# Optimization experiments

Measured on AMD Instinct MI355X. Metric: run time of the kernel, lower is better.

Reference implementation:

```python
import jax, jax.numpy as jnp
import numpy as np

D_MODEL = 512
NUM_HEADS = 8
QUERY_GROUPS = 2
HEAD_DIM = D_MODEL // NUM_HEADS  # 64
ROPE_THETA = 10000.0
SCALE = 0.125  # 1/sqrt(head_dim)
NEG_INF = -1e9


def setup_inputs() -> dict:
    key = jax.random.key(0)
    k1, k2, k3 = jax.random.split(key, 3)
    B, T, S = 2, 512, 16
    x = jax.random.normal(k1, (B, T, S, D_MODEL), jnp.float32)
    padding_mask = jnp.ones((B, T * S), jnp.int32)  # [B, T*H*W], all valid
    qkv_dim = NUM_HEADS * HEAD_DIM + 2 * QUERY_GROUPS * HEAD_DIM  # 768
    qkv_w = jax.random.normal(k2, (qkv_dim, D_MODEL), jnp.float32) / np.float32(np.sqrt(D_MODEL))
    o_w = jax.random.normal(k3, (D_MODEL, NUM_HEADS * HEAD_DIM), jnp.float32) / np.float32(np.sqrt(D_MODEL))
    return {"x": x, "padding_mask": padding_mask, "qkv_w": qkv_w, "o_w": o_w}


def _rope(v, pos):
    # v: [N, T, h, d]; classic RoPE (rotate-half) over temporal positions
    half = v.shape[-1] // 2
    inv_freq = 1.0 / (ROPE_THETA ** (jnp.arange(0, half, dtype=jnp.float32) / half))
    ang = pos[:, None] * inv_freq  # [T, half]
    cos = jnp.cos(ang)[None, :, None, :]
    sin = jnp.sin(ang)[None, :, None, :]
    v1, v2 = v[..., :half], v[..., half:]
    return jnp.concatenate([v1 * cos - v2 * sin, v1 * sin + v2 * cos], axis=-1)


def reference(x, padding_mask, qkv_w, o_w):
    B, T, S, D = x.shape
    # temporal attention: flatten spatial patches into batch -> [B*S, T, D]
    xt = x.transpose(0, 2, 1, 3).reshape(B * S, T, D)
    qkv = xt @ qkv_w.T  # [B*S, T, (H+2G)*hd]
    q_end = NUM_HEADS * HEAD_DIM
    k_end = q_end + QUERY_GROUPS * HEAD_DIM
    q = qkv[..., :q_end].reshape(B * S, T, NUM_HEADS, HEAD_DIM)
    k = qkv[..., q_end:k_end].reshape(B * S, T, QUERY_GROUPS, HEAD_DIM)
    v = qkv[..., k_end:].reshape(B * S, T, QUERY_GROUPS, HEAD_DIM)
    pos = jnp.arange(T, dtype=jnp.float32)
    q = _rope(q, pos)
    k = _rope(k, pos)
    # GQA: broadcast each KV group to its query heads
    rep = NUM_HEADS // QUERY_GROUPS
    k = jnp.repeat(k, rep, axis=2)
    v = jnp.repeat(v, rep, axis=2)
    scores = jnp.einsum('nqhd,nkhd->nhqk', q, k) * SCALE  # [B*S, H, T, T]
    causal = jnp.tril(jnp.ones((T, T), bool))
    pm = padding_mask.astype(bool).reshape(-1, T)  # [B*S, T] query-side mask (as in torch path)
    mask = causal[None, None, :, :] & pm[:, None, :, None]
    scores = jnp.where(mask, scores, NEG_INF)
    attn = jax.nn.softmax(scores, axis=-1)
    out = jnp.einsum('nhqk,nkhd->nqhd', attn, v).reshape(B * S, T, D)
    out = out @ o_w.T  # output projection
    return out.reshape(B, S, T, D).transpose(0, 2, 1, 3)  # back to [B, T, S, D]
```

## Files before the change

kernel.cpp:

```cpp
#include <hip/hip_runtime.h>
#include <hip/hip_bf16.h>

typedef __attribute__((ext_vector_type(8))) short bf16x8;
typedef __attribute__((ext_vector_type(4))) float f32x4;
typedef __attribute__((ext_vector_type(4))) short s16x4;

#define DM 512
#define T_SEQ 512
#define NSEQ 32
#define MROWS 16384
#define QKV_DIM 768
#define HD 64
#define NEG_INF_F (-1000000000.0f)
#define LOG2E 1.44269504088896340736f

__device__ __forceinline__ short f2bf(float f) {
    unsigned int u = __builtin_bit_cast(unsigned int, f);
    unsigned int r = (u + 0x7FFFu + ((u >> 16) & 1u)) >> 16;
    return (short)r;
}

__device__ __forceinline__ short f2bf_hw(float f) {
    __hip_bfloat16 h = __float2bfloat16(f);
    return __builtin_bit_cast(short, h);
}

__device__ __forceinline__ void gload16(const void* g, void* l) {
    __builtin_amdgcn_global_load_lds(
        (const __attribute__((address_space(1))) void*)g,
        (__attribute__((address_space(3))) void*)l, 16, 0, 0);
}

__global__ __launch_bounds__(128) void k_convert(
    const float* __restrict__ x, const float* __restrict__ qkvw, const float* __restrict__ owf,
    short* __restrict__ xt, short* __restrict__ qw, short* __restrict__ ow,
    float* __restrict__ cosT, float* __restrict__ sinT)
{
    int bidx = blockIdx.x, tid = threadIdx.x;
    if (bidx < MROWS) {
        int m = bidx; int n = m >> 9, t = m & 511, b = n >> 4, s = n & 15;
        const float* src = x + ((size_t)((b * 512 + t) * 16 + s)) * 512;
        float4 v = *(const float4*)(src + tid * 4);
        s16x4 o; o.x = f2bf(v.x); o.y = f2bf(v.y); o.z = f2bf(v.z); o.w = f2bf(v.w);
        *(s16x4*)(xt + (size_t)m * 512 + tid * 4) = o;
    } else if (bidx < MROWS + 1280) {
        int wr = bidx - MROWS;
        const float* src; short* dst;
        if (wr < QKV_DIM) { src = qkvw + (size_t)wr * 512; dst = qw + (size_t)wr * 512; }
        else             { src = owf + (size_t)(wr - QKV_DIM) * 512; dst = ow + (size_t)(wr - QKV_DIM) * 512; }
        float4 v = *(const float4*)(src + tid * 4);
        s16x4 o; o.x = f2bf(v.x); o.y = f2bf(v.y); o.z = f2bf(v.z); o.w = f2bf(v.w);
        *(s16x4*)(dst + tid * 4) = o;
    } else {
        int idx = (bidx - (MROWS + 1280)) * 128 + tid;
        int t = idx >> 5, d = idx & 31;
        float inv = powf(10000.0f, -(float)d * (1.0f / 32.0f));
        float ang = (float)t * inv;
        float sv, cv; sincosf(ang, &sv, &cv);
        cosT[idx] = cv; sinT[idx] = sv;
    }
}

__device__ __forceinline__ void gemm_mainloop_db(
    const short* __restrict__ Ab, const short* __restrict__ Bb, int K,
    short* As0, short* As1, short* Bs0, short* Bs1,
    int wave, int lane, f32x4 acc[4][4])
{
    int wr = (wave >> 1) * 64, wc = (wave & 1) * 64;
    int cl = lane & 15, g = lane >> 4;
    auto stg = [&](int kt, short* As, short* Bs) {
        #pragma unroll
        for (int c = 0; c < 2; ++c) {
            int chunk = (wave * 2 + c) * 64 + lane;
            int row = chunk >> 2, kc = chunk & 3;
            gload16(Ab + (size_t)row * K + kt + kc * 8, As + (wave * 2 + c) * 512);
            gload16(Bb + (size_t)row * K + kt + kc * 8, Bs + (wave * 2 + c) * 512);
        }
    };
    stg(0, As0, Bs0);
    for (int kt = 0; kt < K; kt += 32) {
        short* Asc = (kt & 32) ? As1 : As0;
        short* Bsc = (kt & 32) ? Bs1 : Bs0;
        short* Asn = (kt & 32) ? As0 : As1;
        short* Bsn = (kt & 32) ? Bs0 : Bs1;
        __syncthreads();
        if (kt + 32 < K) stg(kt + 32, Asn, Bsn);
        bf16x8 af[4], bg[4];
        #pragma unroll
        for (int mf = 0; mf < 4; ++mf)
            af[mf] = *(const bf16x8*)(Asc + (wr + mf * 16 + cl) * 32 + (g << 3));
        #pragma unroll
        for (int nf = 0; nf < 4; ++nf)
            bg[nf] = *(const bf16x8*)(Bsc + (wc + nf * 16 + cl) * 32 + (g << 3));
        #pragma unroll
        for (int mf = 0; mf < 4; ++mf)
            #pragma unroll
            for (int nf = 0; nf < 4; ++nf)
                acc[mf][nf] = __builtin_amdgcn_mfma_f32_16x16x32_bf16(af[mf], bg[nf], acc[mf][nf], 0, 0, 0);
    }
}

__global__ __launch_bounds__(256) void k_gemm_qkv(
    const short* __restrict__ xt, const short* __restrict__ qw,
    const float* __restrict__ cosT, const float* __restrict__ sinT,
    short* __restrict__ qb, short* __restrict__ kb, short* __restrict__ vtb)
{
    __shared__ short As0[128 * 32], As1[128 * 32], Bs0[128 * 32], Bs1[128 * 32];
    __shared__ short Vld[4][16 * 64];
    int tid = threadIdx.x, wave = tid >> 6, lane = tid & 63;
    int cl = lane & 15, g = lane >> 4;
    int o = blockIdx.x;
    int swz = (o & 7) * 96 + (o >> 3);
    int bm = swz / 6, bn = swz % 6;
    f32x4 acc[4][4] = {};
    gemm_mainloop_db(xt + (size_t)bm * 128 * 512, qw + (size_t)bn * 128 * 512, 512,
                     As0, As1, Bs0, Bs1, wave, lane, acc);

    const float QSC = 0.125f * LOG2E;
    int wr = (wave >> 1) * 64, wc = (wave & 1) * 64;
    int gbase = bn * 128 + wc;

    if (gbase < 640) {
        #pragma unroll
        for (int mf = 0; mf < 4; ++mf) {
            #pragma unroll
            for (int rg = 0; rg < 4; ++rg) {
                int r = bm * 128 + wr + mf * 16 + (g << 2) + rg;
                int n = r >> 9, t = r & 511;
                #pragma unroll
                for (int nf = 0; nf < 2; ++nf) {
                    int dlo = nf * 16 + cl;
                    float v1 = acc[mf][nf][rg];
                    float v2 = acc[mf][nf + 2][rg];
                    float c = cosT[t * 32 + dlo], s = sinT[t * 32 + dlo];
                    if (gbase < 512) {
                        int h = gbase >> 6;
                        size_t base = ((size_t)(n * 8 + h) * 512 + t) * 64;
                        qb[base + dlo]      = f2bf_hw((v1 * c - v2 * s) * QSC);
                        qb[base + dlo + 32] = f2bf_hw((v1 * s + v2 * c) * QSC);
                    } else {
                        int gk = (gbase - 512) >> 6;
                        size_t base = ((size_t)(n * 2 + gk) * 512 + t) * 64;
                        kb[base + dlo]      = f2bf_hw(v1 * c - v2 * s);
                        kb[base + dlo + 32] = f2bf_hw(v1 * s + v2 * c);
                    }
                }
            }
        }
    } else {
        int gq = (gbase - 640) >> 6;
        #pragma unroll
        for (int mf = 0; mf < 4; ++mf) {
            #pragma unroll
            for (int nf = 0; nf < 2; ++nf) {
                int dlo = nf * 16 + cl;
                s16x4 plo, phi;
                #pragma unroll
                for (int rg = 0; rg < 4; ++rg) {
                    ((short*)&plo)[rg] = f2bf_hw(acc[mf][nf][rg]);
                    ((short*)&phi)[rg] = f2bf_hw(acc[mf][nf + 2][rg]);
                }
                *(s16x4*)(&Vld[wave][dlo * 16 + (g << 2)])        = plo;
                *(s16x4*)(&Vld[wave][(dlo + 32) * 16 + (g << 2)]) = phi;
            }
            int r0 = bm * 128 + wr + mf * 16;
            int n = r0 >> 9, t0 = r0 & 511;
            size_t vb = ((size_t)(n * 2 + gq) * 64 + lane) * 512;
            bf16x8 va = *(const bf16x8*)(&Vld[wave][lane * 16]);
            bf16x8 vb8 = *(const bf16x8*)(&Vld[wave][lane * 16 + 8]);
            *(bf16x8*)(vtb + vb + t0)     = va;
            *(bf16x8*)(vtb + vb + t0 + 8) = vb8;
        }
    }
}

__global__ __launch_bounds__(512) void k_attn(
    const short* __restrict__ qb, const short* __restrict__ kb, const short* __restrict__ vtb,
    const int* __restrict__ pm, short* __restrict__ ao)
{
    __shared__ short Kt[2][64 * 64];
    __shared__ short Vt[2][64 * 64];
    __shared__ short Pws[8][16 * 64];
    int tid = threadIdx.x, wave = tid >> 6, lane = tid & 63;
    int cl = lane & 15, g = lane >> 4;
    int o = blockIdx.x;
    int swz = (o & 7) * 64 + (o >> 3);
    int c = swz & 3, hp = (swz >> 2) & 3, n = swz >> 4;
    int kg = hp >> 1;
    int h = hp * 2 + (wave >> 2);
    int u = wave & 3;
    const short* Qb = qb + ((size_t)(n * 8 + h) * 512) * 64;
    const short* Kb = kb + ((size_t)(n * 2 + kg) * 512) * 64;
    const short* Vb = vtb + ((size_t)(n * 2 + kg) * 64) * 512;

    auto stage = [&](int jt, int buf) {
        int c0 = jt * 64;
        int chunk = wave * 64 + lane;
        int row = chunk >> 3, kc = chunk & 7;
        int sw = (kc ^ (row & 7)) << 3;
        gload16(Kb + (size_t)(c0 + row) * 64 + sw, &Kt[buf][wave * 512]);
        gload16(Vb + (size_t)row * 512 + c0 + sw, &Vt[buf][wave * 512]);
    };

    stage(0, 0);
    int buf = 0;
    #pragma unroll
    for (int ph = 0; ph < 2; ++ph) {
        int rowb = (ph ? (7 - c) : c) * 64 + u * 16;
        int NTp = ph ? (8 - c) : (c + 1);
        bf16x8 qf[2];
        #pragma unroll
        for (int ks = 0; ks < 2; ++ks)
            qf[ks] = *(const bf16x8*)(Qb + (size_t)(rowb + cl) * 64 + ks * 32 + (g << 3));
        f32x4 Oc[4] = {};
        float mrow = -1e30f, lrow = 0.f;
        bool rv = pm[n * 512 + rowb + cl] != 0;
        int rq = rowb + cl;

        for (int jt = 0; jt < NTp; ++jt) {
            __syncthreads();
            if (jt + 1 < NTp) stage(jt + 1, buf ^ 1);
            else if (ph == 0) stage(0, buf ^ 1);
            int c0 = jt * 64;
            const short* Kc = Kt[buf];
            const short* Vc = Vt[buf];
            buf ^= 1;

            f32x4 sacc[4] = {};
            #pragma unroll
            for (int ks = 0; ks < 2; ++ks) {
                #pragma unroll
                for (int nf = 0; nf < 4; ++nf) {
                    int row = nf * 16 + cl;
                    int kc = ks * 4 + g;
                    bf16x8 kf = *(const bf16x8*)(Kc + row * 64 + ((kc ^ (row & 7)) << 3));
                    sacc[nf] = __builtin_amdgcn_mfma_f32_16x16x32_bf16(kf, qf[ks], sacc[nf], 0, 0, 0);
                }
            }

            const bool diag = (jt == NTp - 1);
            float rmax = -1e30f;
            if (diag) {
                #pragma unroll
                for (int nf = 0; nf < 4; ++nf)
                    #pragma unroll
                    for (int rg = 0; rg < 4; ++rg) {
                        int kv = c0 + nf * 16 + g * 4 + rg;
                        float sv = sacc[nf][rg];
                        sv = (kv <= rq && rv) ? sv : NEG_INF_F;
                        sacc[nf][rg] = sv;
                        rmax = fmaxf(rmax, sv);
                    }
            } else {
                #pragma unroll
                for (int nf = 0; nf < 4; ++nf)
                    #pragma unroll
                    for (int rg = 0; rg < 4; ++rg)
                        rmax = fmaxf(rmax, sacc[nf][rg]);
            }
            rmax = fmaxf(rmax, __shfl_xor(rmax, 16));
            rmax = fmaxf(rmax, __shfl_xor(rmax, 32));
            float mold = mrow;
            int defer = __all(rmax - mold <= 8.0f);
            float mnew = defer ? mold : fmaxf(mold, rmax);
            mrow = mnew;
            float rsum = 0.f;
            #pragma unroll
            for (int nf = 0; nf < 4; ++nf) {
                s16x4 pk;
                #pragma unroll
                for (int rg = 0; rg < 4; ++rg) {
                    float p = exp2f(sacc[nf][rg] - mnew);
                    rsum += p;
                    ((short*)&pk)[rg] = f2bf_hw(p);
                }
                *(s16x4*)(&Pws[wave][cl * 64 + ((((nf << 1) + (g >> 1)) ^ (cl & 7)) << 3) + ((g & 1) << 2)]) = pk;
            }
            rsum += __shfl_xor(rsum, 16);
            rsum += __shfl_xor(rsum, 32);
            if (defer) {
                lrow += rsum;
            } else {
                float alpha = exp2f(mold - mnew);
                lrow = lrow * alpha + rsum;
                #pragma unroll
                for (int rg = 0; rg < 4; ++rg) {
                    float av = __shfl(alpha, (lane & 48) + (g << 2) + rg);
                    #pragma unroll
                    for (int nf = 0; nf < 4; ++nf) Oc[nf][rg] *= av;
                }
            }

            #pragma unroll
            for (int ks = 0; ks < 2; ++ks) {
                bf16x8 pf = *(const bf16x8*)(&Pws[wave][cl * 64 + (((ks * 4 + g) ^ (cl & 7)) << 3)]);
                #pragma unroll
                for (int nf = 0; nf < 4; ++nf) {
                    int row = nf * 16 + cl;
                    int kc = ks * 4 + g;
                    bf16x8 vf = *(const bf16x8*)(Vc + row * 64 + ((kc ^ (row & 7)) << 3));
                    Oc[nf] = __builtin_amdgcn_mfma_f32_16x16x32_bf16(pf, vf, Oc[nf], 0, 0, 0);
                }
            }
        }

        #pragma unroll
        for (int rg = 0; rg < 4; ++rg) {
            float li = __shfl(lrow, (lane & 48) + (g << 2) + rg);
            float inv = 1.0f / li;
            int r = rowb + g * 4 + rg;
            size_t base = ((size_t)n * 512 + r) * 512 + h * 64;
            #pragma unroll
            for (int nf = 0; nf < 4; ++nf)
                ao[base + nf * 16 + cl] = f2bf_hw(Oc[nf][rg] * inv);
        }
    }
}

__global__ __launch_bounds__(256) void k_gemm_out(
    const short* __restrict__ ao, const short* __restrict__ ow, float* __restrict__ out)
{
    __shared__ short As0[128 * 32], As1[128 * 32], Bs0[128 * 32], Bs1[128 * 32];
    int tid = threadIdx.x, wave = tid >> 6, lane = tid & 63;
    int o = blockIdx.x;
    int swz = (o & 7) * 64 + (o >> 3);
    int bm = swz >> 2, bn = swz & 3;
    f32x4 acc[4][4] = {};
    gemm_mainloop_db(ao + (size_t)bm * 128 * 512, ow + (size_t)bn * 128 * 512, 512,
                     As0, As1, Bs0, Bs1, wave, lane, acc);

    int wr = (wave >> 1) * 64, wc = (wave & 1) * 64;
    #pragma unroll
    for (int mf = 0; mf < 4; ++mf) {
        #pragma unroll
        for (int rg = 0; rg < 4; ++rg) {
            int r = bm * 128 + wr + mf * 16 + ((lane >> 4) << 2) + rg;
            int n = r >> 9, t = r & 511, b = n >> 4, s = n & 15;
            size_t obase = ((size_t)((b * 512 + t) * 16 + s)) * 512;
            #pragma unroll
            for (int nf = 0; nf < 4; ++nf) {
                int ccc = bn * 128 + wc + nf * 16 + (lane & 15);
                out[obase + ccc] = acc[mf][nf][rg];
            }
        }
    }
}

extern "C" void kernel_launch(void* const* d_in, const int* in_sizes, int n_in,
                              void* d_out, int out_size, void* d_ws, size_t ws_size,
                              hipStream_t stream) {
    (void)in_sizes; (void)n_in; (void)out_size; (void)ws_size;
    const float* x    = (const float*)d_in[0];
    const int*   pmsk = (const int*)d_in[1];
    const float* qkvw = (const float*)d_in[2];
    const float* owf  = (const float*)d_in[3];
    char* ws = (char*)d_ws;
    short* xt   = (short*)(ws + 0);
    short* qw   = (short*)(ws + 16777216);
    short* ow   = (short*)(ws + 17563648);
    float* cosT = (float*)(ws + 18087936);
    float* sinT = (float*)(ws + 18153472);
    short* qbuf = (short*)(ws + 18219008);
    short* kbuf = (short*)(ws + 34996224);
    short* vtbuf= (short*)(ws + 39190528);
    short* aobuf = xt;
    float* out = (float*)d_out;

    k_convert<<<dim3(17792), dim3(128), 0, stream>>>(x, qkvw, owf, xt, qw, ow, cosT, sinT);
    k_gemm_qkv<<<dim3(768), dim3(256), 0, stream>>>(xt, qw, cosT, sinT, qbuf, kbuf, vtbuf);
    k_attn<<<dim3(512), dim3(512), 0, stream>>>(qbuf, kbuf, vtbuf, pmsk, aobuf);
    k_gemm_out<<<dim3(512), dim3(256), 0, stream>>>(aobuf, ow, out);
}
```

Baseline: 79.10 us.

## Rewrite QKV GEMM with 256x256 tiles, 8 waves, swizzled LDS, ping-pong pipeline

```diff
diff --git a/kernel.cpp b/kernel.cpp
--- a/kernel.cpp
+++ b/kernel.cpp
@@ -100,32 +100,127 @@
     }
 }
 
-__global__ __launch_bounds__(256) void k_gemm_qkv(
+__global__ __launch_bounds__(512) void k_gemm_qkv(
     const short* __restrict__ xt, const short* __restrict__ qw,
     const float* __restrict__ cosT, const float* __restrict__ sinT,
     short* __restrict__ qb, short* __restrict__ kb, short* __restrict__ vtb)
 {
-    __shared__ short As0[128 * 32], As1[128 * 32], Bs0[128 * 32], Bs1[128 * 32];
-    __shared__ short Vld[4][16 * 64];
+    __shared__ short lds[65536];
     int tid = threadIdx.x, wave = tid >> 6, lane = tid & 63;
     int cl = lane & 15, g = lane >> 4;
     int o = blockIdx.x;
-    int swz = (o & 7) * 96 + (o >> 3);
-    int bm = swz / 6, bn = swz % 6;
-    f32x4 acc[4][4] = {};
-    gemm_mainloop_db(xt + (size_t)bm * 128 * 512, qw + (size_t)bn * 128 * 512, 512,
-                     As0, As1, Bs0, Bs1, wave, lane, acc);
+    int swz = (o & 7) * 24 + (o >> 3);
+    int bm = swz / 3, bn = swz % 3;
+    const short* Ag = xt + (size_t)bm * 256 * 512;
+    const short* Bg = qw + (size_t)bn * 256 * 512;
+
+    int r0 = tid >> 3, kc0 = tid & 7;
+    int r1 = 64 + (tid >> 3);
+    auto stage = [&](int mat, int half, int tile, int buf) {
+        const short* gb = mat ? Bg : Ag;
+        short* lb = lds + mat * 32768 + buf * 16384 + half * 8192;
+        int kt = tile * 64;
+        gload16(gb + (size_t)(half * 128 + r0) * 512 + kt + ((kc0 ^ (r0 & 7)) << 3), lb + tid * 8);
+        gload16(gb + (size_t)(half * 128 + r1) * 512 + kt + ((kc0 ^ (r1 & 7)) << 3), lb + 4096 + tid * 8);
+    };
+
+    stage(1, 0, 0, 0); stage(1, 1, 0, 0); stage(0, 0, 0, 0); stage(0, 1, 0, 0);
+    stage(1, 0, 1, 1); stage(1, 1, 1, 1);
+
+    int wA = (wave >> 2) * 128, wB = (wave & 3) * 64;
+    int cs0 = g ^ (cl & 7);
+    int cs1 = cs0 ^ 4;
+    f32x4 acc[8][4] = {};
+    bf16x8 af[4][2], bg[4][2];
+
+    for (int k = 0; k < 8; ++k) {
+        int buf = k & 1;
+        const short* Ab = lds + buf * 16384;
+        const short* Bb = lds + 32768 + buf * 16384;
+        if (k < 7) stage(0, 0, k + 1, buf ^ 1);
+        asm volatile("s_waitcnt vmcnt(6)" ::: "memory");
+        __builtin_amdgcn_s_barrier();
+        __builtin_amdgcn_sched_barrier(0);
+        #pragma unroll
+        for (int mf = 0; mf < 4; ++mf) {
+            af[mf][0] = *(const bf16x8*)(Ab + (wA + mf * 16 + cl) * 64 + cs0 * 8);
+            af[mf][1] = *(const bf16x8*)(Ab + (wA + mf * 16 + cl) * 64 + cs1 * 8);
+        }
+        #pragma unroll
+        for (int nf = 0; nf < 2; ++nf) {
+            bg[nf][0] = *(const bf16x8*)(Bb + (wB + nf * 16 + cl) * 64 + cs0 * 8);
+            bg[nf][1] = *(const bf16x8*)(Bb + (wB + nf * 16 + cl) * 64 + cs1 * 8);
+        }
+        __builtin_amdgcn_s_setprio(1);
+        #pragma unroll
+        for (int mf = 0; mf < 4; ++mf)
+            #pragma unroll
+            for (int nf = 0; nf < 2; ++nf) {
+                acc[mf][nf] = __builtin_amdgcn_mfma_f32_16x16x32_bf16(af[mf][0], bg[nf][0], acc[mf][nf], 0, 0, 0);
+                acc[mf][nf] = __builtin_amdgcn_mfma_f32_16x16x32_bf16(af[mf][1], bg[nf][1], acc[mf][nf], 0, 0, 0);
+            }
+        __builtin_amdgcn_s_setprio(0);
+        __builtin_amdgcn_s_barrier();
+        __builtin_amdgcn_sched_barrier(0);
+        #pragma unroll
+        for (int nf = 2; nf < 4; ++nf) {
+            bg[nf][0] = *(const bf16x8*)(Bb + (wB + nf * 16 + cl) * 64 + cs0 * 8);
+            bg[nf][1] = *(const bf16x8*)(Bb + (wB + nf * 16 + cl) * 64 + cs1 * 8);
+        }
+        if (k < 7) stage(0, 1, k + 1, buf ^ 1);
+        __builtin_amdgcn_s_setprio(1);
+        #pragma unroll
+        for (int mf = 0; mf < 4; ++mf)
+            #pragma unroll
+            for (int nf = 2; nf < 4; ++nf) {
+                acc[mf][nf] = __builtin_amdgcn_mfma_f32_16x16x32_bf16(af[mf][0], bg[nf][0], acc[mf][nf], 0, 0, 0);
+                acc[mf][nf] = __builtin_amdgcn_mfma_f32_16x16x32_bf16(af[mf][1], bg[nf][1], acc[mf][nf], 0, 0, 0);
+            }
+        __builtin_amdgcn_s_setprio(0);
+        __builtin_amdgcn_s_barrier();
+        __builtin_amdgcn_sched_barrier(0);
+        #pragma unroll
+        for (int mf = 0; mf < 4; ++mf) {
+            af[mf][0] = *(const bf16x8*)(Ab + (wA + 64 + mf * 16 + cl) * 64 + cs0 * 8);
+            af[mf][1] = *(const bf16x8*)(Ab + (wA + 64 + mf * 16 + cl) * 64 + cs1 * 8);
+        }
+        if (k < 6) stage(1, 0, k + 2, buf);
+        __builtin_amdgcn_s_setprio(1);
+        #pragma unroll
+        for (int mf = 0; mf < 4; ++mf)
+            #pragma unroll
+            for (int nf = 0; nf < 2; ++nf) {
+                acc[4 + mf][nf] = __builtin_amdgcn_mfma_f32_16x16x32_bf16(af[mf][0], bg[nf][0], acc[4 + mf][nf], 0, 0, 0);
+                acc[4 + mf][nf] = __builtin_amdgcn_mfma_f32_16x16x32_bf16(af[mf][1], bg[nf][1], acc[4 + mf][nf], 0, 0, 0);
+            }
+        __builtin_amdgcn_s_setprio(0);
+        __builtin_amdgcn_s_barrier();
+        __builtin_amdgcn_sched_barrier(0);
+        if (k < 6) stage(1, 1, k + 2, buf);
+        __builtin_amdgcn_s_setprio(1);
+        #pragma unroll
+        for (int mf = 0; mf < 4; ++mf)
+            #pragma unroll
+            for (int nf = 2; nf < 4; ++nf) {
+                acc[4 + mf][nf] = __builtin_amdgcn_mfma_f32_16x16x32_bf16(af[mf][0], bg[nf][0], acc[4 + mf][nf], 0, 0, 0);
+                acc[4 + mf][nf] = __builtin_amdgcn_mfma_f32_16x16x32_bf16(af[mf][1], bg[nf][1], acc[4 + mf][nf], 0, 0, 0);
+            }
+        __builtin_amdgcn_s_setprio(0);
+        __builtin_amdgcn_s_barrier();
+        __builtin_amdgcn_sched_barrier(0);
+    }
+
+    __syncthreads();
 
     const float QSC = 0.125f * LOG2E;
-    int wr = (wave >> 1) * 64, wc = (wave & 1) * 64;
-    int gbase = bn * 128 + wc;
+    int gbase = bn * 256 + wB;
 
     if (gbase < 640) {
         #pragma unroll
-        for (int mf = 0; mf < 4; ++mf) {
+        for (int mf = 0; mf < 8; ++mf) {
             #pragma unroll
             for (int rg = 0; rg < 4; ++rg) {
-                int r = bm * 128 + wr + mf * 16 + (g << 2) + rg;
+                int r = bm * 256 + wA + mf * 16 + (g << 2) + rg;
                 int n = r >> 9, t = r & 511;
                 #pragma unroll
                 for (int nf = 0; nf < 2; ++nf) {
@@ -149,8 +244,9 @@
         }
     } else {
         int gq = (gbase - 640) >> 6;
-        #pragma unroll
-        for (int mf = 0; mf < 4; ++mf) {
+        short* Vld = lds + wave * 1024;
+        #pragma unroll
+        for (int mf = 0; mf < 8; ++mf) {
             #pragma unroll
             for (int nf = 0; nf < 2; ++nf) {
                 int dlo = nf * 16 + cl;
@@ -160,14 +256,14 @@
                     ((short*)&plo)[rg] = f2bf_hw(acc[mf][nf][rg]);
                     ((short*)&phi)[rg] = f2bf_hw(acc[mf][nf + 2][rg]);
                 }
-                *(s16x4*)(&Vld[wave][dlo * 16 + (g << 2)])        = plo;
-                *(s16x4*)(&Vld[wave][(dlo + 32) * 16 + (g << 2)]) = phi;
-            }
-            int r0 = bm * 128 + wr + mf * 16;
-            int n = r0 >> 9, t0 = r0 & 511;
+                *(s16x4*)(&Vld[dlo * 16 + (g << 2)])        = plo;
+                *(s16x4*)(&Vld[(dlo + 32) * 16 + (g << 2)]) = phi;
+            }
+            int r0v = bm * 256 + wA + mf * 16;
+            int n = r0v >> 9, t0 = r0v & 511;
             size_t vb = ((size_t)(n * 2 + gq) * 64 + lane) * 512;
-            bf16x8 va = *(const bf16x8*)(&Vld[wave][lane * 16]);
-            bf16x8 vb8 = *(const bf16x8*)(&Vld[wave][lane * 16 + 8]);
+            bf16x8 va = *(const bf16x8*)(&Vld[lane * 16]);
+            bf16x8 vb8 = *(const bf16x8*)(&Vld[lane * 16 + 8]);
             *(bf16x8*)(vtb + vb + t0)     = va;
             *(bf16x8*)(vtb + vb + t0 + 8) = vb8;
         }
@@ -367,7 +463,7 @@
     float* out = (float*)d_out;
 
     k_convert<<<dim3(17792), dim3(128), 0, stream>>>(x, qkvw, owf, xt, qw, ow, cosT, sinT);
-    k_gemm_qkv<<<dim3(768), dim3(256), 0, stream>>>(xt, qw, cosT, sinT, qbuf, kbuf, vtbuf);
+    k_gemm_qkv<<<dim3(192), dim3(512), 0, stream>>>(xt, qw, cosT, sinT, qbuf, kbuf, vtbuf);
     k_attn<<<dim3(512), dim3(512), 0, stream>>>(qbuf, kbuf, vtbuf, pmsk, aobuf);
     k_gemm_out<<<dim3(512), dim3(256), 0, stream>>>(aobuf, ow, out);
 }
```

Measured after the change: 81.43 us. 1.03x slower.
